# Kernel optimization log

Measured on AMD Instinct MI355X. Metric: run time of the kernel, lower is better.

Reference implementation:

```python
import jax, jax.numpy as jnp
import numpy as np

B, N = 32, 320          # n_graphs, max_num_nodes
MAX_DIST = 10
NUM_HEADS = 8
AVG_DEG = 8.0


def setup_inputs() -> dict:
    key = jax.random.key(0)
    k1, k2, k3 = jax.random.split(key, 3)
    # random sparse symmetric adjacency, no self loops
    a = jax.random.uniform(k1, (B, N, N)) < (AVG_DEG / N)
    adj = (a | jnp.swapaxes(a, 1, 2)) & ~jnp.eye(N, dtype=bool)[None]
    num_nodes = jax.random.randint(k2, (B,), N // 2 + 1, N + 1).astype(jnp.int32)
    emb_table = jax.random.normal(k3, (MAX_DIST + 2, NUM_HEADS), dtype=jnp.float32)
    emb_table = emb_table.at[0].set(0.0)  # padding_idx=0 (dist == -1 rows)
    return {"adj": adj, "num_nodes": num_nodes, "emb_table": emb_table}


def _batched_apsp(adj, num_nodes, max_dist):
    """Batched all-pairs shortest path distance via parallel frontier BFS.

    adj: [B,N,N] bool, num_nodes: [B] int. Returns dist [B,N,N] int32 with
    -1 for unreachable/padded pairs; reachable dists > max_dist are set to
    max_dist (equivalent after the clamp in the spatial encoder).
    """
    Bn, Nn, _ = adj.shape
    valid = jnp.arange(Nn)[None, :] < num_nodes[:, None]        # [B,N]
    pair = valid[:, :, None] & valid[:, None, :]                # [B,N,N]
    adj = adj & pair
    eye = jnp.eye(Nn, dtype=bool)[None] & pair
    dist = jnp.where(eye, 0, jnp.where(adj, 1, -1)).astype(jnp.int32)
    reach = adj | eye                                           # within dist<=1
    adj_f = adj.astype(jnp.float32)
    for k in range(2, max_dist + 1):
        new_reach = (jnp.matmul(reach.astype(jnp.float32), adj_f) > 0) | reach
        dist = jnp.where(new_reach & ~reach, k, dist)
        reach = new_reach
    # full reachability via distance doubling (handles dist > max_dist)
    full = reach
    steps = int(np.ceil(np.log2(max(Nn / max(max_dist, 1), 2.0))))
    for _ in range(steps):
        f = full.astype(jnp.float32)
        full = jnp.matmul(f, f) > 0
    full = full & pair
    dist = jnp.where(full & (dist < 0), max_dist, dist)
    return jnp.where(pair, dist, -1)


def reference(adj, num_nodes, emb_table):
    dist = _batched_apsp(adj, num_nodes, MAX_DIST)
    # SpatialEncoder: embedding_table(clamp(dist, -1, max_dist) + 1)
    idx = jnp.clip(dist, -1, MAX_DIST) + 1                      # [B,N,N] in [0, max_dist+1]
    return emb_table[idx]                                       # [B,N,N,num_heads]
```

## Files before the change

### kernel.cpp

```cpp
#include <hip/hip_runtime.h>
#include <stdint.h>

typedef unsigned long long u64;
typedef unsigned int u32;
typedef unsigned char u8;

#define Bn 32
#define Nn 320
#define WPN 5
#define MAXD 10
#define NH 8
#define CHS 20
#define NCH (Nn / CHS)
#define TPB Nn
#define ESTR 12
#define ADJ_WORDS (Bn * Nn * WPN)

__device__ __forceinline__ bool detect_byte_mode(const u32* a32) {
    int lane = threadIdx.x & 63;
    u32 or0 = 0, or1 = 0;
    #pragma unroll
    for (int k = 0; k < 16; ++k) {
        u32 v = a32[lane + k * 64];
        or0 |= v & 0x000000FFu;
        or1 |= v & 0x0000FF00u;
    }
    bool a0 = __any(or0 != 0);
    bool a1 = __any(or1 != 0);
    return a0 && a1;
}

__global__ __launch_bounds__(256) void build_adj(
        const u8* __restrict__ a8,
        const int* __restrict__ nn_,
        u64* __restrict__ adjW) {
    bool bytemode = detect_byte_mode((const u32*)a8);
    int t = blockIdx.x * blockDim.x + threadIdx.x;
    if (t >= ADJ_WORDS) return;
    int j = t % Nn;
    int w = (t / Nn) % WPN;
    int b = t / (Nn * WPN);
    int nn = nn_[b];
    u64 bits = 0ull;
    if (j < nn) {
        int jbase = w * 64;
        int lim = nn - jbase; if (lim > 64) lim = 64;
        if (lim > 0) {
            long base = ((long)(b * Nn + j)) * Nn + jbase;
            if (bytemode) {
                const uint4* p = (const uint4*)(a8 + base);
                #pragma unroll
                for (int v = 0; v < 4; ++v) {
                    uint4 x = p[v];
                    u32 n0 = ((x.x & 0x01010101u) * 0x01020408u) >> 24;
                    u32 n1 = ((x.y & 0x01010101u) * 0x01020408u) >> 24;
                    u32 n2 = ((x.z & 0x01010101u) * 0x01020408u) >> 24;
                    u32 n3 = ((x.w & 0x01010101u) * 0x01020408u) >> 24;
                    u64 nib = (u64)((n0 & 0xF) | ((n1 & 0xF) << 4) |
                                    ((n2 & 0xF) << 8) | ((n3 & 0xF) << 12));
                    bits |= nib << (v * 16);
                }
            } else {
                const uint4* p = (const uint4*)(((const u32*)a8) + base);
                #pragma unroll
                for (int v = 0; v < 16; ++v) {
                    uint4 x = p[v];
                    u64 nib = (u64)((x.x != 0u) | ((x.y != 0u) << 1) |
                                    ((x.z != 0u) << 2) | ((x.w != 0u) << 3));
                    bits |= nib << (v * 4);
                }
            }
            if (lim < 64) bits &= (1ull << lim) - 1ull;
        }
    }
    adjW[t] = bits;
}

__global__ __launch_bounds__(TPB) void bfs_write(
        const u64* __restrict__ adjW,
        const int* __restrict__ nn_,
        const float* __restrict__ emb,
        float4* __restrict__ out4) {
    int blk = blockIdx.x;
    int b = blk >> 4;
    int c = blk & 15;
    int t = threadIdx.x;
    int v = t;

    __shared__ __align__(16) u64 adj_s[WPN][Nn];
    __shared__ u32 S[2][Nn];
    __shared__ u8 idx_s[CHS][Nn];
    __shared__ __align__(16) float emb_s[(MAXD + 2) * ESTR];

    if (t < (MAXD + 2) * NH) emb_s[(t >> 3) * ESTR + (t & 7)] = emb[t];

    {
        const uint4* g4 = (const uint4*)(adjW + (size_t)b * (Nn * WPN));
        uint4* d4 = (uint4*)adj_s;
        #pragma unroll
        for (int it = 0; it < 3; ++it) {
            int i = it * TPB + t;
            if (i < (Nn * WPN) / 2) d4[i] = g4[i];
        }
    }
    #pragma unroll
    for (int it = 0; it < 5; ++it) ((u32*)idx_s)[it * TPB + t] = 0;

    int nn = nn_[b];
    int base = c * CHS;

    u32 init = 0;
    if (v >= base && v < base + CHS && v < nn) init = 1u << (v - base);
    S[0][v] = init;

    int vs = nn - base; if (vs > CHS) vs = CHS; if (vs < 0) vs = 0;
    u32 full = (vs >= CHS) ? ((1u << CHS) - 1u) : ((1u << vs) - 1u);

    __syncthreads();
    if (init) idx_s[v - base][v] = 1;

    int p = 0;
    for (int level = 1; level <= Nn; ++level) {
        const u32* Sp = S[p];
        u32 mo = Sp[v];
        u32 acc = mo;
        if (mo != full) {
            #pragma unroll
            for (int w = 0; w < WPN; ++w) {
                u64 m = adj_s[w][v];
                int ubase = w * 64;
                while (m) {
                    int u = ubase + (int)__builtin_ctzll(m);
                    m &= m - 1;
                    acc |= Sp[u];
                }
            }
        }
        u32 nw = acc & ~mo;
        S[p ^ 1][v] = acc;
        if (nw) {
            u8 val = (u8)((level < MAXD ? level : MAXD) + 1);
            u32 m2 = nw;
            while (m2) {
                int s2 = (int)__builtin_ctz(m2);
                m2 &= m2 - 1;
                idx_s[s2][v] = val;
            }
        }
        if (__syncthreads_count(nw != 0) == 0) break;
        p ^= 1;
    }

    float4* gout = out4 + (size_t)(b * Nn + base) * (Nn * NH / 4);
    #pragma unroll
    for (int i = 0; i < 40; ++i) {
        int r = i >> 1;
        int f = ((i & 1) ? Nn : 0) + t;
        int e = idx_s[r][f >> 1];
        const float* ep = emb_s + e * ESTR + ((f & 1) << 2);
        gout[r * (Nn * NH / 4) + f] = *(const float4*)ep;
    }
}

extern "C" void kernel_launch(void* const* d_in, const int* in_sizes, int n_in,
                              void* d_out, int out_size, void* d_ws, size_t ws_size,
                              hipStream_t stream) {
    const u8*    adj = (const u8*)d_in[0];
    const int*   nn  = (const int*)d_in[1];
    const float* emb = (const float*)d_in[2];

    u64* adjW = (u64*)d_ws;

    build_adj<<<ADJ_WORDS / 256, 256, 0, stream>>>(adj, nn, adjW);
    bfs_write<<<Bn * NCH, TPB, 0, stream>>>(adjW, nn, emb, (float4*)d_out);
}
```

Measured before the change: 34.70 us.

## Fuse adjacency packing into BFS, widen source chunks, split embedding write into separate kernel

Adjacency bit-packing now happens inside the BFS kernel, with each thread keeping its own row in registers, so the separate packing kernel and its workspace round trip go away. Each block now tracks 40 BFS sources in 64-bit masks instead of 20, which halves the number of BFS blocks and redundant adjacency reads. The embedding lookup and output write move to a separate fully parallel kernel that reads an index array staged in global memory. This adds roughly 3 MB of index traffic and leaves a BFS phase with fewer blocks, which may reduce occupancy.

Measured after the change: 55.19 us. 59.0% more time.

```diff
diff --git a/kernel.cpp b/kernel.cpp
--- a/kernel.cpp
+++ b/kernel.cpp
@@ -10,11 +10,11 @@
 #define WPN 5
 #define MAXD 10
 #define NH 8
-#define CHS 20
+#define CHS 40
 #define NCH (Nn / CHS)
 #define TPB Nn
 #define ESTR 12
-#define ADJ_WORDS (Bn * Nn * WPN)
+#define IDX_BYTES (Bn * Nn * Nn)
 
 __device__ __forceinline__ bool detect_byte_mode(const u32* a32) {
     int lane = threadIdx.x & 63;
@@ -30,120 +30,102 @@
     return a0 && a1;
 }
 
-__global__ __launch_bounds__(256) void build_adj(
+__global__ __launch_bounds__(TPB) void bfs_idx(
         const u8* __restrict__ a8,
         const int* __restrict__ nn_,
-        u64* __restrict__ adjW) {
+        u8* __restrict__ idxg) {
     bool bytemode = detect_byte_mode((const u32*)a8);
-    int t = blockIdx.x * blockDim.x + threadIdx.x;
-    if (t >= ADJ_WORDS) return;
-    int j = t % Nn;
-    int w = (t / Nn) % WPN;
-    int b = t / (Nn * WPN);
+    int b = blockIdx.x >> 3;
+    int c = blockIdx.x & (NCH - 1);
+    int v = threadIdx.x;
     int nn = nn_[b];
-    u64 bits = 0ull;
-    if (j < nn) {
-        int jbase = w * 64;
-        int lim = nn - jbase; if (lim > 64) lim = 64;
-        if (lim > 0) {
-            long base = ((long)(b * Nn + j)) * Nn + jbase;
-            if (bytemode) {
-                const uint4* p = (const uint4*)(a8 + base);
+
+    __shared__ u64 S[2][Nn];
+    __shared__ __align__(16) u8 idx_s[CHS][Nn];
+
+    #pragma unroll
+    for (int it = 0; it < 10; ++it) ((u32*)idx_s)[it * TPB + v] = 0;
+
+    u64 arow[WPN] = {0, 0, 0, 0, 0};
+    if (v < nn) {
+        if (bytemode) {
+            const uint4* p = (const uint4*)(a8 + (size_t)(b * Nn + v) * Nn);
+            #pragma unroll
+            for (int w = 0; w < WPN; ++w) {
+                u64 bits = 0;
                 #pragma unroll
-                for (int v = 0; v < 4; ++v) {
-                    uint4 x = p[v];
+                for (int q = 0; q < 4; ++q) {
+                    uint4 x = p[w * 4 + q];
                     u32 n0 = ((x.x & 0x01010101u) * 0x01020408u) >> 24;
                     u32 n1 = ((x.y & 0x01010101u) * 0x01020408u) >> 24;
                     u32 n2 = ((x.z & 0x01010101u) * 0x01020408u) >> 24;
                     u32 n3 = ((x.w & 0x01010101u) * 0x01020408u) >> 24;
                     u64 nib = (u64)((n0 & 0xF) | ((n1 & 0xF) << 4) |
                                     ((n2 & 0xF) << 8) | ((n3 & 0xF) << 12));
-                    bits |= nib << (v * 16);
+                    bits |= nib << (q * 16);
                 }
-            } else {
-                const uint4* p = (const uint4*)(((const u32*)a8) + base);
+                arow[w] = bits;
+            }
+        } else {
+            const uint4* p = (const uint4*)(((const u32*)a8) + (size_t)(b * Nn + v) * Nn);
+            #pragma unroll
+            for (int w = 0; w < WPN; ++w) {
+                u64 bits = 0;
                 #pragma unroll
-                for (int v = 0; v < 16; ++v) {
-                    uint4 x = p[v];
+                for (int q = 0; q < 16; ++q) {
+                    uint4 x = p[w * 16 + q];
                     u64 nib = (u64)((x.x != 0u) | ((x.y != 0u) << 1) |
                                     ((x.z != 0u) << 2) | ((x.w != 0u) << 3));
-                    bits |= nib << (v * 4);
+                    bits |= nib << (q * 4);
                 }
+                arow[w] = bits;
             }
-            if (lim < 64) bits &= (1ull << lim) - 1ull;
+        }
+        #pragma unroll
+        for (int w = 0; w < WPN; ++w) {
+            int cc = nn - w * 64;
+            u64 msk = (cc >= 64) ? ~0ull : ((cc <= 0) ? 0ull : ((1ull << cc) - 1ull));
+            arow[w] &= msk;
         }
     }
-    adjW[t] = bits;
-}
 
-__global__ __launch_bounds__(TPB) void bfs_write(
-        const u64* __restrict__ adjW,
-        const int* __restrict__ nn_,
-        const float* __restrict__ emb,
-        float4* __restrict__ out4) {
-    int blk = blockIdx.x;
-    int b = blk >> 4;
-    int c = blk & 15;
-    int t = threadIdx.x;
-    int v = t;
-
-    __shared__ __align__(16) u64 adj_s[WPN][Nn];
-    __shared__ u32 S[2][Nn];
-    __shared__ u8 idx_s[CHS][Nn];
-    __shared__ __align__(16) float emb_s[(MAXD + 2) * ESTR];
-
-    if (t < (MAXD + 2) * NH) emb_s[(t >> 3) * ESTR + (t & 7)] = emb[t];
-
-    {
-        const uint4* g4 = (const uint4*)(adjW + (size_t)b * (Nn * WPN));
-        uint4* d4 = (uint4*)adj_s;
-        #pragma unroll
-        for (int it = 0; it < 3; ++it) {
-            int i = it * TPB + t;
-            if (i < (Nn * WPN) / 2) d4[i] = g4[i];
-        }
-    }
-    #pragma unroll
-    for (int it = 0; it < 5; ++it) ((u32*)idx_s)[it * TPB + t] = 0;
-
-    int nn = nn_[b];
     int base = c * CHS;
-
-    u32 init = 0;
-    if (v >= base && v < base + CHS && v < nn) init = 1u << (v - base);
+    u64 init = 0;
+    if (v >= base && v < base + CHS && v < nn) init = 1ull << (v - base);
     S[0][v] = init;
-
     int vs = nn - base; if (vs > CHS) vs = CHS; if (vs < 0) vs = 0;
-    u32 full = (vs >= CHS) ? ((1u << CHS) - 1u) : ((1u << vs) - 1u);
-
+    u64 full = (1ull << vs) - 1ull;
     __syncthreads();
     if (init) idx_s[v - base][v] = 1;
 
     int p = 0;
     for (int level = 1; level <= Nn; ++level) {
-        const u32* Sp = S[p];
-        u32 mo = Sp[v];
-        u32 acc = mo;
+        const u64* Sp = S[p];
+        u64 mo = Sp[v];
+        u64 acc = mo;
         if (mo != full) {
             #pragma unroll
             for (int w = 0; w < WPN; ++w) {
-                u64 m = adj_s[w][v];
-                int ubase = w * 64;
+                u64 m = arow[w];
+                int ub = w * 64;
                 while (m) {
-                    int u = ubase + (int)__builtin_ctzll(m);
-                    m &= m - 1;
-                    acc |= Sp[u];
+                    int u0 = ub + (int)__builtin_ctzll(m); m &= m - 1;
+                    if (m) {
+                        int u1 = ub + (int)__builtin_ctzll(m); m &= m - 1;
+                        acc |= Sp[u0] | Sp[u1];
+                    } else {
+                        acc |= Sp[u0];
+                    }
                 }
             }
         }
-        u32 nw = acc & ~mo;
+        u64 nw = acc & ~mo;
         S[p ^ 1][v] = acc;
         if (nw) {
             u8 val = (u8)((level < MAXD ? level : MAXD) + 1);
-            u32 m2 = nw;
+            u64 m2 = nw;
             while (m2) {
-                int s2 = (int)__builtin_ctz(m2);
-                m2 &= m2 - 1;
+                int s2 = (int)__builtin_ctzll(m2); m2 &= m2 - 1;
                 idx_s[s2][v] = val;
             }
         }
@@ -151,14 +133,35 @@
         p ^= 1;
     }
 
-    float4* gout = out4 + (size_t)(b * Nn + base) * (Nn * NH / 4);
+    {
+        uint4* dst = (uint4*)(idxg + (size_t)b * (Nn * Nn) + (size_t)base * Nn);
+        const uint4* src = (const uint4*)idx_s;
+        #pragma unroll
+        for (int it = 0; it < 3; ++it) {
+            int i = it * TPB + v;
+            if (i < (CHS * Nn) / 16) dst[i] = src[i];
+        }
+    }
+}
+
+#define K3_TPB 256
+#define K3_PER 10
+#define K3_BLOCKS ((Bn * Nn * Nn * (NH / 4)) / (K3_TPB * K3_PER))
+
+__global__ __launch_bounds__(K3_TPB) void emb_write(
+        const u8* __restrict__ idxg,
+        const float* __restrict__ emb,
+        float4* __restrict__ out4) {
+    __shared__ __align__(16) float emb_s[(MAXD + 2) * ESTR];
+    int t = threadIdx.x;
+    if (t < (MAXD + 2) * NH) emb_s[(t >> 3) * ESTR + (t & 7)] = emb[t];
+    __syncthreads();
+    size_t base = (size_t)blockIdx.x * (K3_TPB * K3_PER);
     #pragma unroll
-    for (int i = 0; i < 40; ++i) {
-        int r = i >> 1;
-        int f = ((i & 1) ? Nn : 0) + t;
-        int e = idx_s[r][f >> 1];
-        const float* ep = emb_s + e * ESTR + ((f & 1) << 2);
-        gout[r * (Nn * NH / 4) + f] = *(const float4*)ep;
+    for (int i = 0; i < K3_PER; ++i) {
+        size_t G = base + (size_t)(i * K3_TPB + t);
+        int e = idxg[G >> 1];
+        out4[G] = *(const float4*)(emb_s + e * ESTR + ((t & 1) << 2));
     }
 }
 
@@ -169,8 +172,8 @@
     const int*   nn  = (const int*)d_in[1];
     const float* emb = (const float*)d_in[2];
 
-    u64* adjW = (u64*)d_ws;
+    u8* idxg = (u8*)d_ws;
 
-    build_adj<<<ADJ_WORDS / 256, 256, 0, stream>>>(adj, nn, adjW);
-    bfs_write<<<Bn * NCH, TPB, 0, stream>>>(adjW, nn, emb, (float4*)d_out);
+    bfs_idx<<<Bn * NCH, TPB, 0, stream>>>(adj, nn, idxg);
+    emb_write<<<K3_BLOCKS, K3_TPB, 0, stream>>>(idxg, emb, (float4*)d_out);
 }
```
